# Kernel optimization log

Hardware: AMD Instinct MI355X
Metric: run time of the kernel (lower is better)

The kernel has to match this reference:

```python
import jax, jax.numpy as jnp
import numpy as np

N_SRC = 50000
N_DST = 10000
E = 1600000
H = 1
F = 128
NEG_SLOPE = 0.2  # GAT default leaky_relu slope


def setup_inputs() -> dict:
    key = jax.random.key(0)
    k1, k2, k3, k4, k5, k6 = jax.random.split(key, 6)
    x_src = jax.random.normal(k1, (N_SRC, H, F), dtype=jnp.float32)
    x_dst = jax.random.normal(k2, (N_DST, H, F), dtype=jnp.float32)
    attn_l = jax.random.normal(k3, (1, H, F), dtype=jnp.float32)
    attn_r = jax.random.normal(k4, (1, H, F), dtype=jnp.float32)
    src_idx = jax.random.randint(k5, (E,), 0, N_SRC, dtype=jnp.int64 if jax.config.jax_enable_x64 else jnp.int32)
    dst_idx = jnp.sort(jax.random.randint(k6, (E,), 0, N_DST, dtype=jnp.int64 if jax.config.jax_enable_x64 else jnp.int32))
    return {"x_src": x_src, "x_dst": x_dst, "attn_l": attn_l, "attn_r": attn_r,
            "src_idx": src_idx, "dst_idx": dst_idx}


def reference(x_src, x_dst, attn_l, attn_r, src_idx, dst_idx):
    n_dst = x_dst.shape[0]
    # per-node attention logits: [N, H]
    el = (x_src * attn_l).sum(axis=-1)
    er = (x_dst * attn_r).sum(axis=-1)
    # per-edge score e = leaky_relu(el[u] + er[v]): [E, H]
    e = jax.nn.leaky_relu(el[src_idx] + er[dst_idx], negative_slope=NEG_SLOPE)
    ex = jnp.exp(e)
    # segment-sum over destination neighborhoods: [N_dst, H]
    sum_ex = jax.ops.segment_sum(ex, dst_idx, num_segments=n_dst)
    attention = ex / sum_ex[dst_idx]  # [E, H]
    # attention-weighted gather of src features, scattered to dst: [N_dst, H, F]
    msg = attention[..., None] * x_src[src_idx]
    out = jax.ops.segment_sum(msg, dst_idx, num_segments=n_dst)
    return out
```

## Files before the change

kernel.cpp:

```cpp
#include <hip/hip_runtime.h>
#include <hip/hip_fp16.h>

#define F 128
#define NEG_SLOPE 0.2f
#define NB 4

#define FMA_MIX_LO(acc, w, h) \
    asm("v_fma_mix_f32 %0, %1, %2, %0 op_sel:[0,0,0] op_sel_hi:[0,1,0]" \
        : "+v"(acc) : "v"(w), "v"(h))
#define FMA_MIX_HI(acc, w, h) \
    asm("v_fma_mix_f32 %0, %1, %2, %0 op_sel:[0,1,0] op_sel_hi:[0,1,0]" \
        : "+v"(acc) : "v"(w), "v"(h))

__global__ __launch_bounds__(256)
void prep_kernel(const float* __restrict__ x_src, const float* __restrict__ attn_l,
                 float* __restrict__ el, __half2* __restrict__ xh, int n_src,
                 const float* __restrict__ x_dst, const float* __restrict__ attn_r,
                 float* __restrict__ er, int n_dst,
                 const int* __restrict__ dst_idx, int* __restrict__ offs, int E,
                 int nlog) {
    if ((int)blockIdx.x < nlog) {
        int wave = blockIdx.x * 4 + (threadIdx.x >> 6);
        int lane = threadIdx.x & 63;
        int half = lane >> 5;
        int l32  = lane & 31;
        int row  = wave * 2 + half;
        const float* x; const float* attn; float* o; int r; bool is_src;
        if (row < n_src)              { x = x_src; attn = attn_l; o = el; r = row; is_src = true; }
        else if (row < n_src + n_dst) { x = x_dst; attn = attn_r; o = er; r = row - n_src; is_src = false; }
        else return;
        float4 xv = reinterpret_cast<const float4*>(x)[(size_t)r * 32 + l32];
        float4 av = reinterpret_cast<const float4*>(attn)[l32];
        if (xh && is_src) {
            __half2 h0 = __floats2half2_rn(xv.x, xv.y);
            __half2 h1 = __floats2half2_rn(xv.z, xv.w);
            uint2 u;
            u.x = *reinterpret_cast<unsigned int*>(&h0);
            u.y = *reinterpret_cast<unsigned int*>(&h1);
            reinterpret_cast<uint2*>(xh)[(size_t)r * 32 + l32] = u;
        }
        float s = xv.x * av.x + xv.y * av.y + xv.z * av.z + xv.w * av.w;
        #pragma unroll
        for (int o_ = 16; o_ > 0; o_ >>= 1) s += __shfl_xor(s, o_, 64);
        if (l32 == 0) o[r] = s;
    } else {
        int e = ((int)blockIdx.x - nlog) * 256 + threadIdx.x;
        if (e >= E) return;
        int d = dst_idx[e];
        int prev = (e == 0) ? -1 : dst_idx[e - 1];
        for (int v = prev + 1; v <= d; ++v) offs[v] = e;
        if (e == E - 1)
            for (int v = d + 1; v <= n_dst; ++v) offs[v] = E;
    }
}

__global__ __launch_bounds__(256)
void reorder_kernel(const int* __restrict__ src_idx, const int* __restrict__ offs,
                    const float* __restrict__ el, const float* __restrict__ er,
                    int2* __restrict__ ew, int* __restrict__ boffs,
                    int n_dst, float inv_bdiv) {
    int v = blockIdx.x * 4 + (threadIdx.x >> 6);
    if (v >= n_dst) return;
    int lane = threadIdx.x & 63;
    int start = offs[v], end = offs[v + 1];
    float erv = er[v];
    unsigned long long lt = (1ULL << lane) - 1ULL;

    int c0 = 0, c1 = 0, c2 = 0, c3 = 0;
    for (int base = start; base < end; base += 64) {
        int e = base + lane;
        int b = -1;
        if (e < end) {
            int s = src_idx[e];
            b = (int)((float)s * inv_bdiv);
            if (b > NB - 1) b = NB - 1;
        }
        c0 += __popcll(__ballot(b == 0));
        c1 += __popcll(__ballot(b == 1));
        c2 += __popcll(__ballot(b == 2));
        c3 += __popcll(__ballot(b == 3));
    }
    int base0 = start;
    int base1 = base0 + c0;
    int base2 = base1 + c1;
    int base3 = base2 + c2;
    if (lane == 0) {
        boffs[(size_t)v * (NB + 1) + 0] = base0;
        boffs[(size_t)v * (NB + 1) + 1] = base1;
        boffs[(size_t)v * (NB + 1) + 2] = base2;
        boffs[(size_t)v * (NB + 1) + 3] = base3;
        boffs[(size_t)v * (NB + 1) + 4] = base3 + c3;
    }

    for (int base = start; base < end; base += 64) {
        int e = base + lane;
        int b = -1, s = 0;
        float w = 0.f;
        if (e < end) {
            s = src_idx[e];
            b = (int)((float)s * inv_bdiv);
            if (b > NB - 1) b = NB - 1;
            float l = el[s] + erv;
            l = l > 0.f ? l : NEG_SLOPE * l;
            w = __expf(l);
        }
        int2 payload = make_int2(s * (F / 8), __float_as_int(w));
        unsigned long long m;
        m = __ballot(b == 0);
        if (b == 0) ew[base0 + __popcll(m & lt)] = payload;
        base0 += __popcll(m);
        m = __ballot(b == 1);
        if (b == 1) ew[base1 + __popcll(m & lt)] = payload;
        base1 += __popcll(m);
        m = __ballot(b == 2);
        if (b == 2) ew[base2 + __popcll(m & lt)] = payload;
        base2 += __popcll(m);
        m = __ballot(b == 3);
        if (b == 3) ew[base3 + __popcll(m & lt)] = payload;
        base3 += __popcll(m);
    }
}

__global__ __launch_bounds__(256)
void agg_slice_kernel(const __half2* __restrict__ xh,
                      const int2* __restrict__ ew,
                      const int* __restrict__ boffs,
                      float* __restrict__ part, float* __restrict__ pden,
                      int n_dst) {
    int b = blockIdx.x & (NB - 1);
    int v = ((int)blockIdx.x >> 2) * 4 + (threadIdx.x >> 6);
    if (v >= n_dst) return;
    int lane = threadIdx.x & 63;
    int g    = lane >> 4;
    int l16  = lane & 15;

    int s0e = boffs[(size_t)v * (NB + 1) + b];
    int s1e = boffs[(size_t)v * (NB + 1) + b + 1];

    const float4* x4h = reinterpret_cast<const float4*>(xh);

    float a0[8], a1[8];
    #pragma unroll
    for (int k = 0; k < 8; ++k) { a0[k] = 0.f; a1[k] = 0.f; }
    float d0 = 0.f, d1 = 0.f;

    int count = s1e - s0e;
    int full  = count & ~7;
    for (int it = 0; it < full; it += 8) {
        int2 q0 = ew[s0e + it + g];
        int2 q1 = ew[s0e + it + 4 + g];
        float w0 = __int_as_float(q0.y);
        float w1 = __int_as_float(q1.y);
        d0 += w0; d1 += w1;
        float4 r0 = x4h[q0.x + l16];
        float4 r1 = x4h[q1.x + l16];
        const unsigned int* u0 = reinterpret_cast<const unsigned int*>(&r0);
        const unsigned int* u1 = reinterpret_cast<const unsigned int*>(&r1);
        #pragma unroll
        for (int k = 0; k < 4; ++k) {
            FMA_MIX_LO(a0[2*k],   w0, u0[k]);
            FMA_MIX_HI(a0[2*k+1], w0, u0[k]);
            FMA_MIX_LO(a1[2*k],   w1, u1[k]);
            FMA_MIX_HI(a1[2*k+1], w1, u1[k]);
        }
    }
    for (int e = s0e + full + g; e < s1e; e += 4) {
        int2 q = ew[e];
        float w = __int_as_float(q.y);
        d0 += w;
        float4 r = x4h[q.x + l16];
        const unsigned int* u = reinterpret_cast<const unsigned int*>(&r);
        #pragma unroll
        for (int k = 0; k < 4; ++k) {
            FMA_MIX_LO(a0[2*k],   w, u[k]);
            FMA_MIX_HI(a0[2*k+1], w, u[k]);
        }
    }
    #pragma unroll
    for (int k = 0; k < 8; ++k) a0[k] += a1[k];
    d0 += d1;

    #pragma unroll
    for (int k = 0; k < 8; ++k) {
        a0[k] += __shfl_xor(a0[k], 16, 64);
        a0[k] += __shfl_xor(a0[k], 32, 64);
    }
    d0 += __shfl_xor(d0, 16, 64);
    d0 += __shfl_xor(d0, 32, 64);

    if (g == 0) {
        float4* pp = reinterpret_cast<float4*>(&part[((size_t)b * n_dst + v) * F + l16 * 8]);
        pp[0] = make_float4(a0[0], a0[1], a0[2], a0[3]);
        pp[1] = make_float4(a0[4], a0[5], a0[6], a0[7]);
        if (l16 == 0) pden[(size_t)b * n_dst + v] = d0;
    }
}

__global__ __launch_bounds__(256)
void combine_kernel(const float* __restrict__ part, const float* __restrict__ pden,
                    float* __restrict__ out, int n_dst) {
    int t = blockIdx.x * 256 + threadIdx.x;
    int total = n_dst * (F / 4);
    if (t >= total) return;
    int v = t >> 5;
    const float4* p4 = reinterpret_cast<const float4*>(part);
    float4 n = make_float4(0.f, 0.f, 0.f, 0.f);
    float den = 0.f;
    #pragma unroll
    for (int b = 0; b < NB; ++b) {
        float4 u = p4[(size_t)b * total + t];
        n.x += u.x; n.y += u.y; n.z += u.z; n.w += u.w;
        den += pden[(size_t)b * n_dst + v];
    }
    float inv = (den > 0.f) ? 1.f / den : 0.f;
    reinterpret_cast<float4*>(out)[t] = make_float4(n.x*inv, n.y*inv, n.z*inv, n.w*inv);
}

template<bool H>
__global__ __launch_bounds__(256)
void agg_full_kernel(const __half2* __restrict__ xh, const float* __restrict__ x_src,
                     const float* __restrict__ el, const float* __restrict__ er,
                     const int* __restrict__ src_idx, const int* __restrict__ offs,
                     float* __restrict__ out, int n_dst) {
    int v = blockIdx.x * 4 + (threadIdx.x >> 6);
    if (v >= n_dst) return;
    int lane = threadIdx.x & 63;
    int g    = lane >> 4;
    int l16  = lane & 15;

    int start = offs[v];
    int end   = offs[v + 1];
    int count = end - start;
    float erv = er[v];

    const float4* x4h = reinterpret_cast<const float4*>(xh);
    const float4* x4f = reinterpret_cast<const float4*>(x_src);

    float a0[8];
    #pragma unroll
    for (int k = 0; k < 8; ++k) a0[k] = 0.f;
    float d0 = 0.f;

    for (int e = start + g; e < end; e += 4) {
        int s = src_idx[e];
        float l = el[s] + erv;
        l = l > 0.f ? l : NEG_SLOPE * l;
        float w = __expf(l);
        d0 += w;
        if (H) {
            float4 r = x4h[(size_t)s * (F / 8) + l16];
            const unsigned int* u = reinterpret_cast<const unsigned int*>(&r);
            #pragma unroll
            for (int k = 0; k < 4; ++k) {
                FMA_MIX_LO(a0[2*k],   w, u[k]);
                FMA_MIX_HI(a0[2*k+1], w, u[k]);
            }
        } else {
            float4 p = x4f[(size_t)s * (F/4) + l16*2];
            float4 q = x4f[(size_t)s * (F/4) + l16*2 + 1];
            a0[0]+=w*p.x; a0[1]+=w*p.y; a0[2]+=w*p.z; a0[3]+=w*p.w;
            a0[4]+=w*q.x; a0[5]+=w*q.y; a0[6]+=w*q.z; a0[7]+=w*q.w;
        }
    }
    #pragma unroll
    for (int k = 0; k < 8; ++k) {
        a0[k] += __shfl_xor(a0[k], 16, 64);
        a0[k] += __shfl_xor(a0[k], 32, 64);
    }
    d0 += __shfl_xor(d0, 16, 64);
    d0 += __shfl_xor(d0, 32, 64);

    if (g == 0) {
        float inv = (count > 0) ? 1.f / d0 : 0.f;
        float4* dst = reinterpret_cast<float4*>(&out[(size_t)v * F + l16 * 8]);
        dst[0] = make_float4(a0[0]*inv, a0[1]*inv, a0[2]*inv, a0[3]*inv);
        dst[1] = make_float4(a0[4]*inv, a0[5]*inv, a0[6]*inv, a0[7]*inv);
    }
}

extern "C" void kernel_launch(void* const* d_in, const int* in_sizes, int n_in,
                              void* d_out, int out_size, void* d_ws, size_t ws_size,
                              hipStream_t stream) {
    const float* x_src   = (const float*)d_in[0];
    const float* x_dst   = (const float*)d_in[1];
    const float* attn_l  = (const float*)d_in[2];
    const float* attn_r  = (const float*)d_in[3];
    const int*   src_idx = (const int*)d_in[4];
    const int*   dst_idx = (const int*)d_in[5];

    int n_src = in_sizes[0] / F;
    int n_dst = in_sizes[1] / F;
    int E     = in_sizes[4];

    float* out  = (float*)d_out;
    float* el   = (float*)d_ws;
    float* er   = el + n_src;
    int*   offs = (int*)(er + n_dst);
    uintptr_t p = (uintptr_t)(offs + n_dst + 1);
    p = (p + 15) & ~(uintptr_t)15;
    __half2* xh = (__half2*)p;
    uintptr_t q = p + (size_t)n_src * F * sizeof(__half);
    q = (q + 15) & ~(uintptr_t)15;
    int2*  ew    = (int2*)q;
    int*   boffs = (int*)(ew + E);
    uintptr_t r  = (uintptr_t)(boffs + (size_t)n_dst * (NB + 1));
    r = (r + 15) & ~(uintptr_t)15;
    float* part  = (float*)r;
    float* pden  = part + (size_t)NB * n_dst * F;

    size_t need_fp16 = (q - (uintptr_t)d_ws);
    size_t need_full = ((uintptr_t)(pden + (size_t)NB * n_dst)) - (uintptr_t)d_ws;
    bool fp16ok = ws_size >= need_fp16;
    bool fullok = ws_size >= need_full;

    int nlog = (n_src + n_dst + 7) / 8;
    int noff = (E + 255) / 256;
    prep_kernel<<<nlog + noff, 256, 0, stream>>>(
        x_src, attn_l, el, fp16ok ? xh : nullptr, n_src,
        x_dst, attn_r, er, n_dst, dst_idx, offs, E, nlog);

    if (fullok && fp16ok) {
        int bdiv = (n_src + NB - 1) / NB;
        float inv_bdiv = 1.0f / (float)bdiv;
        reorder_kernel<<<(n_dst + 3) / 4, 256, 0, stream>>>(
            src_idx, offs, el, er, ew, boffs, n_dst, inv_bdiv);
        int ngrp = (n_dst + 3) / 4;
        agg_slice_kernel<<<ngrp * NB, 256, 0, stream>>>(
            xh, ew, boffs, part, pden, n_dst);
        combine_kernel<<<(n_dst * (F / 4) + 255) / 256, 256, 0, stream>>>(
            part, pden, out, n_dst);
    } else if (fp16ok) {
        agg_full_kernel<true><<<(n_dst + 3) / 4, 256, 0, stream>>>(
            xh, nullptr, el, er, src_idx, offs, out, n_dst);
    } else {
        agg_full_kernel<false><<<(n_dst + 3) / 4, 256, 0, stream>>>(
            nullptr, x_src, el, er, src_idx, offs, out, n_dst);
    }
}
```

Measured before the change: 72.65 us.

## Map one 16-lane group per destination slice in aggregation kernel

Aggregation work is remapped so each 16-lane group handles a whole (destination, bucket) slice serially, instead of a full 64-lane wave splitting the slice's edges across four groups. This removes the cross-group shuffle reduction and gives each wave four independent destinations, with the edge loop unrolled by four for memory-level parallelism. In exchange, each group walks its edges serially with a single accumulator chain, which lengthens the FMA dependency chain and can cause load imbalance between lanes of a wave when slice sizes differ.

```diff
diff --git a/kernel.cpp b/kernel.cpp
--- a/kernel.cpp
+++ b/kernel.cpp
@@ -127,73 +127,70 @@
                       const int* __restrict__ boffs,
                       float* __restrict__ part, float* __restrict__ pden,
                       int n_dst) {
-    int b = blockIdx.x & (NB - 1);
-    int v = ((int)blockIdx.x >> 2) * 4 + (threadIdx.x >> 6);
+    int b   = blockIdx.x & (NB - 1);
+    int v   = ((int)blockIdx.x >> 2) * 16 + (threadIdx.x >> 4);
     if (v >= n_dst) return;
-    int lane = threadIdx.x & 63;
-    int g    = lane >> 4;
-    int l16  = lane & 15;
+    int l16 = threadIdx.x & 15;
 
     int s0e = boffs[(size_t)v * (NB + 1) + b];
     int s1e = boffs[(size_t)v * (NB + 1) + b + 1];
 
     const float4* x4h = reinterpret_cast<const float4*>(xh);
 
-    float a0[8], a1[8];
+    float a[8];
     #pragma unroll
-    for (int k = 0; k < 8; ++k) { a0[k] = 0.f; a1[k] = 0.f; }
-    float d0 = 0.f, d1 = 0.f;
-
-    int count = s1e - s0e;
-    int full  = count & ~7;
-    for (int it = 0; it < full; it += 8) {
-        int2 q0 = ew[s0e + it + g];
-        int2 q1 = ew[s0e + it + 4 + g];
+    for (int k = 0; k < 8; ++k) a[k] = 0.f;
+    float den = 0.f;
+
+    int cnt  = s1e - s0e;
+    int full = cnt & ~3;
+    for (int it = 0; it < full; it += 4) {
+        int2 q0 = ew[s0e + it];
+        int2 q1 = ew[s0e + it + 1];
+        int2 q2 = ew[s0e + it + 2];
+        int2 q3 = ew[s0e + it + 3];
         float w0 = __int_as_float(q0.y);
         float w1 = __int_as_float(q1.y);
-        d0 += w0; d1 += w1;
+        float w2 = __int_as_float(q2.y);
+        float w3 = __int_as_float(q3.y);
         float4 r0 = x4h[q0.x + l16];
         float4 r1 = x4h[q1.x + l16];
+        float4 r2 = x4h[q2.x + l16];
+        float4 r3 = x4h[q3.x + l16];
+        den += w0 + w1 + w2 + w3;
         const unsigned int* u0 = reinterpret_cast<const unsigned int*>(&r0);
         const unsigned int* u1 = reinterpret_cast<const unsigned int*>(&r1);
+        const unsigned int* u2 = reinterpret_cast<const unsigned int*>(&r2);
+        const unsigned int* u3 = reinterpret_cast<const unsigned int*>(&r3);
         #pragma unroll
         for (int k = 0; k < 4; ++k) {
-            FMA_MIX_LO(a0[2*k],   w0, u0[k]);
-            FMA_MIX_HI(a0[2*k+1], w0, u0[k]);
-            FMA_MIX_LO(a1[2*k],   w1, u1[k]);
-            FMA_MIX_HI(a1[2*k+1], w1, u1[k]);
-        }
-    }
-    for (int e = s0e + full + g; e < s1e; e += 4) {
-        int2 q = ew[e];
+            FMA_MIX_LO(a[2*k],   w0, u0[k]);
+            FMA_MIX_HI(a[2*k+1], w0, u0[k]);
+            FMA_MIX_LO(a[2*k],   w1, u1[k]);
+            FMA_MIX_HI(a[2*k+1], w1, u1[k]);
+            FMA_MIX_LO(a[2*k],   w2, u2[k]);
+            FMA_MIX_HI(a[2*k+1], w2, u2[k]);
+            FMA_MIX_LO(a[2*k],   w3, u3[k]);
+            FMA_MIX_HI(a[2*k+1], w3, u3[k]);
+        }
+    }
+    for (int it = full; it < cnt; ++it) {
+        int2 q = ew[s0e + it];
         float w = __int_as_float(q.y);
-        d0 += w;
+        den += w;
         float4 r = x4h[q.x + l16];
         const unsigned int* u = reinterpret_cast<const unsigned int*>(&r);
         #pragma unroll
         for (int k = 0; k < 4; ++k) {
-            FMA_MIX_LO(a0[2*k],   w, u[k]);
-            FMA_MIX_HI(a0[2*k+1], w, u[k]);
-        }
-    }
-    #pragma unroll
-    for (int k = 0; k < 8; ++k) a0[k] += a1[k];
-    d0 += d1;
-
-    #pragma unroll
-    for (int k = 0; k < 8; ++k) {
-        a0[k] += __shfl_xor(a0[k], 16, 64);
-        a0[k] += __shfl_xor(a0[k], 32, 64);
-    }
-    d0 += __shfl_xor(d0, 16, 64);
-    d0 += __shfl_xor(d0, 32, 64);
-
-    if (g == 0) {
-        float4* pp = reinterpret_cast<float4*>(&part[((size_t)b * n_dst + v) * F + l16 * 8]);
-        pp[0] = make_float4(a0[0], a0[1], a0[2], a0[3]);
-        pp[1] = make_float4(a0[4], a0[5], a0[6], a0[7]);
-        if (l16 == 0) pden[(size_t)b * n_dst + v] = d0;
-    }
+            FMA_MIX_LO(a[2*k],   w, u[k]);
+            FMA_MIX_HI(a[2*k+1], w, u[k]);
+        }
+    }
+
+    float4* pp = reinterpret_cast<float4*>(&part[((size_t)b * n_dst + v) * F + l16 * 8]);
+    pp[0] = make_float4(a[0], a[1], a[2], a[3]);
+    pp[1] = make_float4(a[4], a[5], a[6], a[7]);
+    if (l16 == 0) pden[(size_t)b * n_dst + v] = den;
 }
 
 __global__ __launch_bounds__(256)
@@ -324,8 +321,8 @@
         float inv_bdiv = 1.0f / (float)bdiv;
         reorder_kernel<<<(n_dst + 3) / 4, 256, 0, stream>>>(
             src_idx, offs, el, er, ew, boffs, n_dst, inv_bdiv);
-        int ngrp = (n_dst + 3) / 4;
-        agg_slice_kernel<<<ngrp * NB, 256, 0, stream>>>(
+        int nblk = ((n_dst + 15) / 16) * NB;
+        agg_slice_kernel<<<nblk, 256, 0, stream>>>(
             xh, ew, boffs, part, pden, n_dst);
         combine_kernel<<<(n_dst * (F / 4) + 255) / 256, 256, 0, stream>>>(
             part, pden, out, n_dst);
```

New measurement: 73.69 us. About the same (+1.4%).
